# Optimization experiments

Hardware: AMD Instinct MI355X
Metric: run time of the kernel (lower is better)

Reference implementation:

```python
import jax, jax.numpy as jnp
import numpy as np

NUM_HEADS = 16
EMB_DIM = 1024
HEAD_DIM = EMB_DIM // NUM_HEADS


def setup_inputs() -> dict:
    key = jax.random.key(0)
    k1, k2, k3, k4 = jax.random.split(key, 4)
    B, S = 2, 2048
    X = jax.random.normal(k1, (B, S, EMB_DIM), dtype=jnp.float32)
    # torch Linear(in, out, bias=False): y = x @ W.T ; store as [in, out]
    Wq = jax.random.normal(k2, (EMB_DIM, EMB_DIM), dtype=jnp.float32) * (EMB_DIM ** -0.5)
    Wk = jax.random.normal(k3, (EMB_DIM, HEAD_DIM), dtype=jnp.float32) * (EMB_DIM ** -0.5)
    Wv = jax.random.normal(k4, (EMB_DIM, HEAD_DIM), dtype=jnp.float32) * (EMB_DIM ** -0.5)
    return {"X": X, "Wq": Wq, "Wk": Wk, "Wv": Wv}


def reference(X, Wq, Wk, Wv):
    B, S, E = X.shape
    H, D = NUM_HEADS, HEAD_DIM
    q = (X @ Wq).reshape(B, S, H, D).transpose(0, 2, 1, 3)  # [B,H,S,D]
    k = X @ Wk  # [B,S,D] shared K head
    v = X @ Wv  # [B,S,D] shared V head
    scores = jnp.einsum('bhsd,btd->bhst', q, k) / jnp.sqrt(jnp.float32(D))
    causal = jnp.tril(jnp.ones((S, S), dtype=bool))
    scores = jnp.where(causal, scores, -jnp.inf)
    probs = jax.nn.softmax(scores, axis=-1)  # [B,H,S,S]
    out = jnp.einsum('bhst,btd->bhsd', probs, v)  # [B,H,S,D]
    return out.transpose(0, 2, 1, 3).reshape(B, S, E)
```

## Files before the change

### kernel.cpp

```cpp
#include <hip/hip_runtime.h>
#include <stdint.h>

#define NH   16
#define EMB  1024
#define HD   64
#define BSZ  2
#define SEQ  2048
#define NROW (BSZ * SEQ)

typedef __attribute__((ext_vector_type(8))) short bf16x8;
typedef __attribute__((ext_vector_type(4))) float f32x4;

__device__ __forceinline__ uint16_t f2bf(float f) {
    union { float f; uint32_t i; } v; v.f = f;
    uint32_t r = v.i + 0x7FFFu + ((v.i >> 16) & 1u);
    return (uint16_t)(r >> 16);
}
__device__ __forceinline__ uint32_t pack2(float a, float b) {
    return (uint32_t)f2bf(a) | ((uint32_t)f2bf(b) << 16);
}
__device__ __forceinline__ uint32_t pack2r(float a, float b) {
    union { float f; uint32_t i; } ua, ub; ua.f = a; ub.f = b;
    return ((ua.i + 0x8000u) >> 16) | ((ub.i + 0x8000u) & 0xFFFF0000u);
}

__device__ __forceinline__ void gl2lds16(const uint16_t* g, uint16_t* l) {
    __builtin_amdgcn_global_load_lds(
        static_cast<const uint32_t*>(static_cast<const void*>(g)),
        static_cast<uint32_t*>(static_cast<void*>(l)), 16, 0, 0);
}

__global__ __launch_bounds__(256) void prep(
    const float* __restrict__ X, uint16_t* __restrict__ Xbf,
    const float* __restrict__ Wq, const float* __restrict__ Wk,
    const float* __restrict__ Wv, uint16_t* __restrict__ Wqt,
    uint16_t* __restrict__ Wkt, uint16_t* __restrict__ Wvt)
{
    __shared__ uint16_t T[64][72];
    const int tid = threadIdx.x;
    if (blockIdx.x < 2048) {
        size_t idx = ((size_t)blockIdx.x * 256 + tid) * 8;
        float4 a = *(const float4*)&X[idx];
        float4 b = *(const float4*)&X[idx + 4];
        *(uint4*)&Xbf[idx] = make_uint4(pack2(a.x, a.y), pack2(a.z, a.w),
                                        pack2(b.x, b.y), pack2(b.z, b.w));
        return;
    }
    const int id = blockIdx.x - 2048;
    const float* W; uint16_t* Wt; int k0, n0, ldw;
    if (id < 256)      { W = Wq; Wt = Wqt; k0 = (id >> 4) * 64; n0 = (id & 15) * 64; ldw = EMB; }
    else if (id < 272) { W = Wk; Wt = Wkt; k0 = (id - 256) * 64; n0 = 0; ldw = HD; }
    else               { W = Wv; Wt = Wvt; k0 = (id - 272) * 64; n0 = 0; ldw = HD; }

    const int r = tid >> 2, c4 = (tid & 3) * 16;
#pragma unroll
    for (int i = 0; i < 4; ++i) {
        float4 wv = *(const float4*)&W[(size_t)(k0 + r) * ldw + n0 + c4 + 4 * i];
        T[r][c4 + 4 * i + 0] = f2bf(wv.x); T[r][c4 + 4 * i + 1] = f2bf(wv.y);
        T[r][c4 + 4 * i + 2] = f2bf(wv.z); T[r][c4 + 4 * i + 3] = f2bf(wv.w);
    }
    __syncthreads();
    const int n = tid >> 2, kk = (tid & 3) * 16;
    uint32_t o[8];
#pragma unroll
    for (int i = 0; i < 8; ++i)
        o[i] = (uint32_t)T[kk + 2 * i][n] | ((uint32_t)T[kk + 2 * i + 1][n] << 16);
    uint16_t* dst = &Wt[(size_t)(n0 + n) * EMB + k0 + kk];
    *(uint4*)dst       = make_uint4(o[0], o[1], o[2], o[3]);
    *(uint4*)(dst + 8) = make_uint4(o[4], o[5], o[6], o[7]);
}

__global__ __launch_bounds__(256) void qkv_gemm_mfma4(
    const uint16_t* __restrict__ Xbf, const uint16_t* __restrict__ Wqt,
    const uint16_t* __restrict__ Wkt, const uint16_t* __restrict__ Wvt,
    float* __restrict__ Qout, uint16_t* __restrict__ Kbf,
    uint16_t* __restrict__ Vtbf)
{
    const int tid  = threadIdx.x;
    const int w    = tid >> 6, lane = tid & 63;
    const int l    = lane & 15, quad = lane >> 4;
    const int wm   = w & 1, wn = w >> 1;
    const int nt   = blockIdx.x;
    const int m0   = blockIdx.y * 128;

    __shared__ uint16_t As[2][128 * 32];
    __shared__ uint16_t Bs[2][128 * 32];

    const uint16_t* gA[2]; uint32_t ldsA[2];
    const uint16_t* gB[2]; uint32_t ldsB[2];
#pragma unroll
    for (int i = 0; i < 2; ++i) {
        int ch = (w * 2 + i) * 64 + lane;
        int r = ch >> 2, cp = ch & 3;
        int c = cp ^ ((r >> 1) & 3);
        gA[i] = &Xbf[(size_t)(m0 + r) * EMB + c * 8];
        ldsA[i] = (w * 2 + i) * 512;
        const uint16_t* bs;
        if (nt < 8)      bs = &Wqt[(size_t)(nt * 128 + r) * EMB + c * 8];
        else if (r < 64) bs = &Wkt[(size_t)r * EMB + c * 8];
        else             bs = &Wvt[(size_t)(r - 64) * EMB + c * 8];
        gB[i] = bs;
        ldsB[i] = (w * 2 + i) * 512;
    }

    uint32_t offA[4], offB[4];
#pragma unroll
    for (int i = 0; i < 4; ++i) {
        int row = 64 * wm + 16 * i + l;
        offA[i] = (row * 4 + (quad ^ ((row >> 1) & 3))) * 8;
    }
#pragma unroll
    for (int j = 0; j < 4; ++j) {
        int row = 64 * wn + 16 * j + l;
        offB[j] = (row * 4 + (quad ^ ((row >> 1) & 3))) * 8;
    }

    f32x4 acc[4][4] = {};

    gl2lds16(gA[0], &As[0][ldsA[0]]);
    gl2lds16(gA[1], &As[0][ldsA[1]]);
    gl2lds16(gB[0], &Bs[0][ldsB[0]]);
    gl2lds16(gB[1], &Bs[0][ldsB[1]]);
    gA[0] += 32; gA[1] += 32; gB[0] += 32; gB[1] += 32;
    __syncthreads();

    for (int ks = 0; ks < 32; ++ks) {
        const int cur = ks & 1, nxt = cur ^ 1;
        if (ks < 31) {
            gl2lds16(gA[0], &As[nxt][ldsA[0]]);
            gl2lds16(gA[1], &As[nxt][ldsA[1]]);
            gl2lds16(gB[0], &Bs[nxt][ldsB[0]]);
            gl2lds16(gB[1], &Bs[nxt][ldsB[1]]);
            gA[0] += 32; gA[1] += 32; gB[0] += 32; gB[1] += 32;
        }
        bf16x8 af[4], bf[4];
#pragma unroll
        for (int i = 0; i < 4; ++i) af[i] = *(const bf16x8*)&As[cur][offA[i]];
#pragma unroll
        for (int j = 0; j < 4; ++j) bf[j] = *(const bf16x8*)&Bs[cur][offB[j]];
#pragma unroll
        for (int i = 0; i < 4; ++i)
#pragma unroll
            for (int j = 0; j < 4; ++j)
                acc[i][j] = __builtin_amdgcn_mfma_f32_16x16x32_bf16(
                    af[i], bf[j], acc[i][j], 0, 0, 0);
        __syncthreads();
    }

    if (nt < 8) {
#pragma unroll
        for (int i = 0; i < 4; ++i)
#pragma unroll
            for (int j = 0; j < 4; ++j)
#pragma unroll
                for (int r = 0; r < 4; ++r)
                    Qout[(size_t)(m0 + 64 * wm + 16 * i + 4 * quad + r) * EMB
                         + nt * 128 + 64 * wn + 16 * j + l] = acc[i][j][r];
    } else if (wn == 0) {
#pragma unroll
        for (int i = 0; i < 4; ++i)
#pragma unroll
            for (int j = 0; j < 4; ++j)
#pragma unroll
                for (int r = 0; r < 4; ++r)
                    Kbf[(size_t)(m0 + 64 * wm + 16 * i + 4 * quad + r) * HD
                        + 16 * j + l] = f2bf(acc[i][j][r]);
    } else {
#pragma unroll
        for (int i = 0; i < 4; ++i)
#pragma unroll
            for (int j = 0; j < 4; ++j)
#pragma unroll
                for (int r = 0; r < 4; ++r)
                    Vtbf[(size_t)(16 * j + l) * NROW
                         + m0 + 64 * wm + 16 * i + 4 * quad + r] = f2bf(acc[i][j][r]);
    }
}

__global__ __launch_bounds__(256) void mqa_attn(
    const uint16_t* __restrict__ Kbf, const uint16_t* __restrict__ Vtbf,
    float* __restrict__ Out)
{
    const int tid  = threadIdx.x;
    const int w    = tid >> 6;
    const int lane = tid & 63;
    const int l    = lane & 15;
    const int quad = lane >> 4;
    const int i  = blockIdx.x;
    const int h  = blockIdx.y, b = blockIdx.z;
    const int qt[2] = {31 - i, i};
    const int q0[2] = {qt[0] * 64, qt[1] * 64};

    __shared__ __align__(16) uint16_t KV[2][64][72];
    __shared__ __align__(16) uint16_t Ps[2][64][72];

    const float C = 0.125f * 1.4426950408889634f;
    const int sr = tid >> 2, sc = (tid & 3) * 16;

#pragma unroll
    for (int t = 0; t < 2; ++t) {
        const float* src = &Out[(size_t)(b * SEQ + q0[t] + sr) * EMB + h * HD + sc];
        float4 f0 = *(const float4*)(src + 0);
        float4 f1 = *(const float4*)(src + 4);
        float4 f2 = *(const float4*)(src + 8);
        float4 f3 = *(const float4*)(src + 12);
        *(uint4*)&Ps[t][sr][sc] =
            make_uint4(pack2(f0.x * C, f0.y * C), pack2(f0.z * C, f0.w * C),
                       pack2(f1.x * C, f1.y * C), pack2(f1.z * C, f1.w * C));
        *(uint4*)&Ps[t][sr][sc + 8] =
            make_uint4(pack2(f2.x * C, f2.y * C), pack2(f2.z * C, f2.w * C),
                       pack2(f3.x * C, f3.y * C), pack2(f3.z * C, f3.w * C));
    }

    uint4 kg0, kg1, vg0, vg1;
    {
        const uint4* ks = (const uint4*)&Kbf[(size_t)(b * SEQ + sr) * HD + sc];
        kg0 = ks[0]; kg1 = ks[1];
        const uint4* vs = (const uint4*)&Vtbf[(size_t)sr * NROW + b * SEQ + sc];
        vg0 = vs[0]; vg1 = vs[1];
    }
    __syncthreads();

    bf16x8 qf[2][2];
#pragma unroll
    for (int t = 0; t < 2; ++t) {
        qf[t][0] = *(const bf16x8*)&Ps[t][16 * w + l][quad * 8];
        qf[t][1] = *(const bf16x8*)&Ps[t][16 * w + l][32 + quad * 8];
    }

    float lsum[2] = {0.f, 0.f};
    f32x4 accO[2][4] = {};
    const int qi_l = 16 * w + l;

    for (int kb = 0; kb <= qt[0]; ++kb) {
        __syncthreads();
        *(uint4*)&KV[0][sr][sc]     = kg0;
        *(uint4*)&KV[0][sr][sc + 8] = kg1;
        *(uint4*)&KV[1][sr][sc]     = vg0;
        *(uint4*)&KV[1][sr][sc + 8] = vg1;
        __syncthreads();

        if (kb < qt[0]) {
            const int k0n = (kb + 1) * 64;
            const uint4* ks = (const uint4*)&Kbf[(size_t)(b * SEQ + k0n + sr) * HD + sc];
            kg0 = ks[0]; kg1 = ks[1];
            const uint4* vs = (const uint4*)&Vtbf[(size_t)sr * NROW + b * SEQ + k0n + sc];
            vg0 = vs[0]; vg1 = vs[1];
        }

        const bool doB = (kb <= qt[1]);

        bf16x8 ka[4][2];
#pragma unroll
        for (int ts = 0; ts < 4; ++ts) {
            ka[ts][0] = *(const bf16x8*)&KV[0][16 * ts + l][quad * 8];
            ka[ts][1] = *(const bf16x8*)&KV[0][16 * ts + l][32 + quad * 8];
        }
#pragma unroll
        for (int t = 0; t < 2; ++t) {
            if (t == 1 && !doB) break;
            f32x4 accS[4] = {};
#pragma unroll
            for (int ts = 0; ts < 4; ++ts) {
                accS[ts] = __builtin_amdgcn_mfma_f32_16x16x32_bf16(ka[ts][0], qf[t][0], accS[ts], 0, 0, 0);
                accS[ts] = __builtin_amdgcn_mfma_f32_16x16x32_bf16(ka[ts][1], qf[t][1], accS[ts], 0, 0, 0);
            }
            float pv[16];
#pragma unroll
            for (int ts = 0; ts < 4; ++ts)
#pragma unroll
                for (int r = 0; r < 4; ++r)
                    pv[4 * ts + r] = exp2f(accS[ts][r]);
            if (kb == qt[t]) {
#pragma unroll
                for (int ts = 0; ts < 4; ++ts)
#pragma unroll
                    for (int r = 0; r < 4; ++r)
                        if ((16 * ts + 4 * quad + r) > qi_l) pv[4 * ts + r] = 0.f;
            }
            float s = 0.f;
#pragma unroll
            for (int j = 0; j < 16; ++j) s += pv[j];
            lsum[t] += s;
#pragma unroll
            for (int ts = 0; ts < 4; ++ts)
                *(uint2*)&Ps[t][16 * w + l][16 * ts + 4 * quad] =
                    make_uint2(pack2r(pv[4 * ts + 0], pv[4 * ts + 1]),
                               pack2r(pv[4 * ts + 2], pv[4 * ts + 3]));
        }

        bf16x8 vb[4][2];
#pragma unroll
        for (int tn = 0; tn < 4; ++tn) {
            vb[tn][0] = *(const bf16x8*)&KV[1][16 * tn + l][quad * 8];
            vb[tn][1] = *(const bf16x8*)&KV[1][16 * tn + l][32 + quad * 8];
        }
#pragma unroll
        for (int t = 0; t < 2; ++t) {
            if (t == 1 && !doB) break;
            bf16x8 pa0 = *(const bf16x8*)&Ps[t][16 * w + l][quad * 8];
            bf16x8 pa1 = *(const bf16x8*)&Ps[t][16 * w + l][32 + quad * 8];
#pragma unroll
            for (int tn = 0; tn < 4; ++tn) {
                accO[t][tn] = __builtin_amdgcn_mfma_f32_16x16x32_bf16(pa0, vb[tn][0], accO[t][tn], 0, 0, 0);
                accO[t][tn] = __builtin_amdgcn_mfma_f32_16x16x32_bf16(pa1, vb[tn][1], accO[t][tn], 0, 0, 0);
            }
        }
    }

#pragma unroll
    for (int t = 0; t < 2; ++t) {
        float s = lsum[t];
        s += __shfl_xor(s, 16);
        s += __shfl_xor(s, 32);
        float inv = 1.0f / s;
#pragma unroll
        for (int r = 0; r < 4; ++r) {
            float invr = __shfl(inv, (quad << 2) + r);
            const int row = q0[t] + 16 * w + 4 * quad + r;
#pragma unroll
            for (int tn = 0; tn < 4; ++tn)
                Out[(size_t)(b * SEQ + row) * EMB + h * HD + 16 * tn + l] =
                    accO[t][tn][r] * invr;
        }
    }
}

__global__ __launch_bounds__(256) void qkv_gemm_vec(
    const float* __restrict__ X,  const float* __restrict__ Wq,
    const float* __restrict__ Wk, const float* __restrict__ Wv,
    float* __restrict__ Qout, uint16_t* __restrict__ Kbf,
    uint16_t* __restrict__ Vtbf)
{
    const int tid = threadIdx.x;
    const int tx = tid & 15, ty = tid >> 4;
    const int bx = blockIdx.x;
    const int m0 = blockIdx.y * 64;

    const float* W; int ldw, n0;
    if (bx < 16)       { W = Wq; ldw = EMB; n0 = bx * 64; }
    else if (bx == 16) { W = Wk; ldw = HD;  n0 = 0; }
    else               { W = Wv; ldw = HD;  n0 = 0; }

    __shared__ float sA[64][17];
    __shared__ float sB[16][64];

    float acc[4][4] = {};
    const int arow = tid >> 2, acol = (tid & 3) * 4;
    const int brow = tid >> 4, bcol = (tid & 15) * 4;

    for (int k0 = 0; k0 < EMB; k0 += 16) {
        float4 fa = *(const float4*)&X[(size_t)(m0 + arow) * EMB + k0 + acol];
        float4 fb = *(const float4*)&W[(size_t)(k0 + brow) * ldw + n0 + bcol];
        sA[arow][acol + 0] = fa.x; sA[arow][acol + 1] = fa.y;
        sA[arow][acol + 2] = fa.z; sA[arow][acol + 3] = fa.w;
        sB[brow][bcol + 0] = fb.x; sB[brow][bcol + 1] = fb.y;
        sB[brow][bcol + 2] = fb.z; sB[brow][bcol + 3] = fb.w;
        __syncthreads();
#pragma unroll
        for (int kk = 0; kk < 16; ++kk) {
            float a0 = sA[4 * ty + 0][kk];
            float a1 = sA[4 * ty + 1][kk];
            float a2 = sA[4 * ty + 2][kk];
            float a3 = sA[4 * ty + 3][kk];
            float4 bq = *(const float4*)&sB[kk][4 * tx];
            acc[0][0] += a0 * bq.x; acc[0][1] += a0 * bq.y; acc[0][2] += a0 * bq.z; acc[0][3] += a0 * bq.w;
            acc[1][0] += a1 * bq.x; acc[1][1] += a1 * bq.y; acc[1][2] += a1 * bq.z; acc[1][3] += a1 * bq.w;
            acc[2][0] += a2 * bq.x; acc[2][1] += a2 * bq.y; acc[2][2] += a2 * bq.z; acc[2][3] += a2 * bq.w;
            acc[3][0] += a3 * bq.x; acc[3][1] += a3 * bq.y; acc[3][2] += a3 * bq.z; acc[3][3] += a3 * bq.w;
        }
        __syncthreads();
    }

    if (bx < 16) {
#pragma unroll
        for (int i = 0; i < 4; ++i)
            *(float4*)&Qout[(size_t)(m0 + 4 * ty + i) * EMB + n0 + 4 * tx] =
                make_float4(acc[i][0], acc[i][1], acc[i][2], acc[i][3]);
    } else if (bx == 16) {
#pragma unroll
        for (int i = 0; i < 4; ++i) {
            ushort4 u; u.x = f2bf(acc[i][0]); u.y = f2bf(acc[i][1]);
            u.z = f2bf(acc[i][2]); u.w = f2bf(acc[i][3]);
            *(ushort4*)&Kbf[(size_t)(m0 + 4 * ty + i) * HD + 4 * tx] = u;
        }
    } else {
#pragma unroll
        for (int j = 0; j < 4; ++j) {
            ushort4 u; u.x = f2bf(acc[0][j]); u.y = f2bf(acc[1][j]);
            u.z = f2bf(acc[2][j]); u.w = f2bf(acc[3][j]);
            *(ushort4*)&Vtbf[(size_t)(4 * tx + j) * NROW + m0 + 4 * ty] = u;
        }
    }
}

extern "C" void kernel_launch(void* const* d_in, const int* in_sizes, int n_in,
                              void* d_out, int out_size, void* d_ws, size_t ws_size,
                              hipStream_t stream) {
    const float* X  = (const float*)d_in[0];
    const float* Wq = (const float*)d_in[1];
    const float* Wk = (const float*)d_in[2];
    const float* Wv = (const float*)d_in[3];
    float* OutP = (float*)d_out;

    char* ws = (char*)d_ws;
    const size_t MB = 1024 * 1024;
    uint16_t* Xbf  = (uint16_t*)(ws);
    uint16_t* Wqt  = (uint16_t*)(ws + 8 * MB);
    uint16_t* Wkt  = (uint16_t*)(ws + 10 * MB);
    uint16_t* Wvt  = (uint16_t*)(ws + 10 * MB + 256 * 1024);
    uint16_t* Kbf  = (uint16_t*)(ws + 10 * MB + 512 * 1024);
    uint16_t* Vtbf = (uint16_t*)(ws + 11 * MB);

    if (ws_size >= 12 * MB) {
        prep<<<2336, 256, 0, stream>>>(X, Xbf, Wq, Wk, Wv, Wqt, Wkt, Wvt);
        qkv_gemm_mfma4<<<dim3(9, 32), 256, 0, stream>>>(Xbf, Wqt, Wkt, Wvt,
                                                        OutP, Kbf, Vtbf);
        mqa_attn<<<dim3(16, NH, BSZ), 256, 0, stream>>>(Kbf, Vtbf, OutP);
    } else {
        uint16_t* KbfS  = (uint16_t*)d_ws;
        uint16_t* VtbfS = KbfS + (size_t)NROW * HD;
        qkv_gemm_vec<<<dim3(18, 64), 256, 0, stream>>>(X, Wq, Wk, Wv, OutP, KbfS, VtbfS);
        mqa_attn<<<dim3(16, NH, BSZ), 256, 0, stream>>>(KbfS, VtbfS, OutP);
    }
}
```

Measured before the change: 153.3 us.

## Double-buffer K/V in LDS, compute row sums via MFMA, use hardware bf16 pack

Measured after the change: 150.4 us. About the same (-1.9%).

```diff
diff --git a/kernel.cpp b/kernel.cpp
--- a/kernel.cpp
+++ b/kernel.cpp
@@ -19,9 +19,10 @@
 __device__ __forceinline__ uint32_t pack2(float a, float b) {
     return (uint32_t)f2bf(a) | ((uint32_t)f2bf(b) << 16);
 }
-__device__ __forceinline__ uint32_t pack2r(float a, float b) {
-    union { float f; uint32_t i; } ua, ub; ua.f = a; ub.f = b;
-    return ((ua.i + 0x8000u) >> 16) | ((ub.i + 0x8000u) & 0xFFFF0000u);
+__device__ __forceinline__ uint32_t cvtpk(float a, float b) {
+    uint32_t r;
+    asm("v_cvt_pk_bf16_f32 %0, %1, %2" : "=v"(r) : "v"(a), "v"(b));
+    return r;
 }
 
 __device__ __forceinline__ void gl2lds16(const uint16_t* g, uint16_t* l) {
@@ -191,7 +192,7 @@
     const int qt[2] = {31 - i, i};
     const int q0[2] = {qt[0] * 64, qt[1] * 64};
 
-    __shared__ __align__(16) uint16_t KV[2][64][72];
+    __shared__ __align__(16) uint16_t KV[2][2][64][72];
     __shared__ __align__(16) uint16_t Ps[2][64][72];
 
     const float C = 0.125f * 1.4426950408889634f;
@@ -219,6 +220,16 @@
         const uint4* vs = (const uint4*)&Vtbf[(size_t)sr * NROW + b * SEQ + sc];
         vg0 = vs[0]; vg1 = vs[1];
     }
+    *(uint4*)&KV[0][0][sr][sc]     = kg0;
+    *(uint4*)&KV[0][0][sr][sc + 8] = kg1;
+    *(uint4*)&KV[0][1][sr][sc]     = vg0;
+    *(uint4*)&KV[0][1][sr][sc + 8] = vg1;
+    {
+        const uint4* ks = (const uint4*)&Kbf[(size_t)(b * SEQ + 64 + sr) * HD + sc];
+        kg0 = ks[0]; kg1 = ks[1];
+        const uint4* vs = (const uint4*)&Vtbf[(size_t)sr * NROW + b * SEQ + 64 + sc];
+        vg0 = vs[0]; vg1 = vs[1];
+    }
     __syncthreads();
 
     bf16x8 qf[2][2];
@@ -228,34 +239,40 @@
         qf[t][1] = *(const bf16x8*)&Ps[t][16 * w + l][32 + quad * 8];
     }
 
-    float lsum[2] = {0.f, 0.f};
+    bf16x8 ones;
+#pragma unroll
+    for (int j = 0; j < 8; ++j) ones[j] = (short)0x3F80;
+
     f32x4 accO[2][4] = {};
+    f32x4 accSum[2] = {};
     const int qi_l = 16 * w + l;
 
     for (int kb = 0; kb <= qt[0]; ++kb) {
-        __syncthreads();
-        *(uint4*)&KV[0][sr][sc]     = kg0;
-        *(uint4*)&KV[0][sr][sc + 8] = kg1;
-        *(uint4*)&KV[1][sr][sc]     = vg0;
-        *(uint4*)&KV[1][sr][sc + 8] = vg1;
-        __syncthreads();
+        const int cur = kb & 1, nxt = cur ^ 1;
+
+        bf16x8 ka[4][2];
+#pragma unroll
+        for (int ts = 0; ts < 4; ++ts) {
+            ka[ts][0] = *(const bf16x8*)&KV[cur][0][16 * ts + l][quad * 8];
+            ka[ts][1] = *(const bf16x8*)&KV[cur][0][16 * ts + l][32 + quad * 8];
+        }
 
         if (kb < qt[0]) {
-            const int k0n = (kb + 1) * 64;
-            const uint4* ks = (const uint4*)&Kbf[(size_t)(b * SEQ + k0n + sr) * HD + sc];
-            kg0 = ks[0]; kg1 = ks[1];
-            const uint4* vs = (const uint4*)&Vtbf[(size_t)sr * NROW + b * SEQ + k0n + sc];
-            vg0 = vs[0]; vg1 = vs[1];
+            *(uint4*)&KV[nxt][0][sr][sc]     = kg0;
+            *(uint4*)&KV[nxt][0][sr][sc + 8] = kg1;
+            *(uint4*)&KV[nxt][1][sr][sc]     = vg0;
+            *(uint4*)&KV[nxt][1][sr][sc + 8] = vg1;
+            if (kb + 1 < qt[0]) {
+                const int k0n = (kb + 2) * 64;
+                const uint4* ks = (const uint4*)&Kbf[(size_t)(b * SEQ + k0n + sr) * HD + sc];
+                kg0 = ks[0]; kg1 = ks[1];
+                const uint4* vs = (const uint4*)&Vtbf[(size_t)sr * NROW + b * SEQ + k0n + sc];
+                vg0 = vs[0]; vg1 = vs[1];
+            }
         }
 
         const bool doB = (kb <= qt[1]);
 
-        bf16x8 ka[4][2];
-#pragma unroll
-        for (int ts = 0; ts < 4; ++ts) {
-            ka[ts][0] = *(const bf16x8*)&KV[0][16 * ts + l][quad * 8];
-            ka[ts][1] = *(const bf16x8*)&KV[0][16 * ts + l][32 + quad * 8];
-        }
 #pragma unroll
         for (int t = 0; t < 2; ++t) {
             if (t == 1 && !doB) break;
@@ -278,22 +295,18 @@
                     for (int r = 0; r < 4; ++r)
                         if ((16 * ts + 4 * quad + r) > qi_l) pv[4 * ts + r] = 0.f;
             }
-            float s = 0.f;
-#pragma unroll
-            for (int j = 0; j < 16; ++j) s += pv[j];
-            lsum[t] += s;
 #pragma unroll
             for (int ts = 0; ts < 4; ++ts)
                 *(uint2*)&Ps[t][16 * w + l][16 * ts + 4 * quad] =
-                    make_uint2(pack2r(pv[4 * ts + 0], pv[4 * ts + 1]),
-                               pack2r(pv[4 * ts + 2], pv[4 * ts + 3]));
+                    make_uint2(cvtpk(pv[4 * ts + 0], pv[4 * ts + 1]),
+                               cvtpk(pv[4 * ts + 2], pv[4 * ts + 3]));
         }
 
         bf16x8 vb[4][2];
 #pragma unroll
         for (int tn = 0; tn < 4; ++tn) {
-            vb[tn][0] = *(const bf16x8*)&KV[1][16 * tn + l][quad * 8];
-            vb[tn][1] = *(const bf16x8*)&KV[1][16 * tn + l][32 + quad * 8];
+            vb[tn][0] = *(const bf16x8*)&KV[cur][1][16 * tn + l][quad * 8];
+            vb[tn][1] = *(const bf16x8*)&KV[cur][1][16 * tn + l][32 + quad * 8];
         }
 #pragma unroll
         for (int t = 0; t < 2; ++t) {
@@ -305,18 +318,18 @@
                 accO[t][tn] = __builtin_amdgcn_mfma_f32_16x16x32_bf16(pa0, vb[tn][0], accO[t][tn], 0, 0, 0);
                 accO[t][tn] = __builtin_amdgcn_mfma_f32_16x16x32_bf16(pa1, vb[tn][1], accO[t][tn], 0, 0, 0);
             }
-        }
+            accSum[t] = __builtin_amdgcn_mfma_f32_16x16x32_bf16(pa0, ones, accSum[t], 0, 0, 0);
+            accSum[t] = __builtin_amdgcn_mfma_f32_16x16x32_bf16(pa1, ones, accSum[t], 0, 0, 0);
+        }
+
+        __syncthreads();
     }
 
 #pragma unroll
     for (int t = 0; t < 2; ++t) {
-        float s = lsum[t];
-        s += __shfl_xor(s, 16);
-        s += __shfl_xor(s, 32);
-        float inv = 1.0f / s;
 #pragma unroll
         for (int r = 0; r < 4; ++r) {
-            float invr = __shfl(inv, (quad << 2) + r);
+            float invr = 1.0f / accSum[t][r];
             const int row = q0[t] + 16 * w + 4 * quad + r;
 #pragma unroll
             for (int tn = 0; tn < 4; ++tn)
```
